# Kernel tuning notes

Hardware: AMD Instinct MI355X
Metric: run time of the kernel (lower is better)

## Reference

```python
import jax, jax.numpy as jnp
import numpy as np

B, H, W, C = 16, 56, 56, 384
WS, SHIFT, NH = 8, 4, 12
HID = 4 * C
N = WS * WS
EPS = 1e-5


def _rel_index():
    coords = np.stack(np.meshgrid(np.arange(WS), np.arange(WS), indexing='ij')).reshape(2, -1)
    rel = coords[:, :, None] - coords[:, None, :]
    rel = rel.transpose(1, 2, 0).astype(np.int32)
    rel[..., 0] += WS - 1
    rel[..., 1] += WS - 1
    rel[..., 0] *= 2 * WS - 1
    return rel.sum(-1)  # [N, N]


def _attn_mask():
    img = np.zeros((H, W))
    bounds = [(0, H - WS), (H - WS, H - SHIFT), (H - SHIFT, H)]
    cnt = 0
    for h0, h1 in bounds:
        for w0, w1 in bounds:
            img[h0:h1, w0:w1] = cnt
            cnt += 1
    mw = img.reshape(H // WS, WS, W // WS, WS).transpose(0, 2, 1, 3).reshape(-1, N)
    am = mw[:, None, :] - mw[:, :, None]
    return np.where(am != 0, -100.0, 0.0).astype(np.float32)  # [nW, N, N]


def setup_inputs() -> dict:
    key = jax.random.key(0)
    ks = jax.random.split(key, 12)
    s = lambda k, shp, sc=0.02: (jax.random.normal(k, shp, jnp.float32) * sc)
    return {
        'x': jax.random.normal(ks[0], (B, H * W, C), jnp.float32),
        'norm1_g': jnp.ones((C,), jnp.float32),
        'norm1_b': jnp.zeros((C,), jnp.float32),
        'qkv_w': s(ks[1], (C, 3 * C)),
        'qkv_b': jnp.zeros((3 * C,), jnp.float32),
        'proj_w': s(ks[2], (C, C)),
        'proj_b': jnp.zeros((C,), jnp.float32),
        'rel_bias': s(ks[3], ((2 * WS - 1) * (2 * WS - 1), NH)),
        'norm2_g': jnp.ones((C,), jnp.float32),
        'norm2_b': jnp.zeros((C,), jnp.float32),
        'fc1_w': s(ks[4], (C, HID)),
        'fc1_b': jnp.zeros((HID,), jnp.float32),
        'fc2_w': s(ks[5], (HID, C)),
        'fc2_b': jnp.zeros((C,), jnp.float32),
        'rel_index': jnp.asarray(_rel_index()),
        'attn_mask': jnp.asarray(_attn_mask()),
    }


def _ln(x, g, b):
    mu = x.mean(-1, keepdims=True)
    var = ((x - mu) ** 2).mean(-1, keepdims=True)
    return (x - mu) * jax.lax.rsqrt(var + EPS) * g + b


def reference(x, norm1_g, norm1_b, qkv_w, qkv_b, proj_w, proj_b, rel_bias,
              norm2_g, norm2_b, fc1_w, fc1_b, fc2_w, fc2_b, rel_index, attn_mask):
    hd = C // NH
    scale = hd ** -0.5
    shortcut = x
    h = _ln(x, norm1_g, norm1_b).reshape(B, H, W, C)
    h = jnp.roll(h, (-SHIFT, -SHIFT), axis=(1, 2))
    # window partition -> [B*nW, N, C]
    xw = h.reshape(B, H // WS, WS, W // WS, WS, C).transpose(0, 1, 3, 2, 4, 5).reshape(-1, N, C)
    B_ = xw.shape[0]
    qkv = (xw @ qkv_w + qkv_b).reshape(B_, N, 3, NH, hd).transpose(2, 0, 3, 1, 4)
    q, k, v = qkv[0], qkv[1], qkv[2]  # [B_, NH, N, hd]
    attn = jnp.einsum('bhid,bhjd->bhij', q * scale, k)
    bias = rel_bias[rel_index.reshape(-1)].reshape(N, N, NH).transpose(2, 0, 1)  # [NH, N, N]
    attn = attn + bias[None]
    nW = attn_mask.shape[0]
    attn = attn.reshape(B_ // nW, nW, NH, N, N) + attn_mask[None, :, None]
    attn = attn.reshape(B_, NH, N, N)
    attn = jax.nn.softmax(attn, axis=-1)
    out = jnp.einsum('bhij,bhjd->bhid', attn, v).transpose(0, 2, 1, 3).reshape(B_, N, C)
    out = out @ proj_w + proj_b
    # window reverse
    out = out.reshape(B, H // WS, W // WS, WS, WS, C).transpose(0, 1, 3, 2, 4, 5).reshape(B, H, W, C)
    out = jnp.roll(out, (SHIFT, SHIFT), axis=(1, 2)).reshape(B, H * W, C)
    y = shortcut + out
    h2 = _ln(y, norm2_g, norm2_b)
    mlp = jax.nn.gelu(h2 @ fc1_w + fc1_b, approximate=False) @ fc2_w + fc2_b
    y = y + mlp
    return (y, attn)
```

## Files before the change

### kernel.cpp

```cpp
#include <hip/hip_runtime.h>
#include <hip/hip_bf16.h>
#include <math.h>

#define ROWS 50176

typedef short s16;
typedef unsigned int u32;
typedef __attribute__((ext_vector_type(4))) float f32x4;
typedef __attribute__((ext_vector_type(8))) short s16x8;
typedef __attribute__((ext_vector_type(8))) __bf16 bf16x8;

typedef __attribute__((address_space(1))) const u32 gu32;
typedef __attribute__((address_space(3))) u32 lu32;

__device__ __forceinline__ void gload16(const void* g, void* l) {
  __builtin_amdgcn_global_load_lds((gu32*)g, (lu32*)l, 16, 0, 0);
}

__device__ __forceinline__ s16 f2bf(float f) {
  unsigned u = __float_as_uint(f);
  u = (u + 0x7fffu + ((u >> 16) & 1u)) >> 16;
  return (s16)u;
}

__global__ void convT(const float* __restrict__ src, s16* __restrict__ dst, int K, int N) {
  int i = blockIdx.x * 256 + threadIdx.x;
  if (i >= K * N) return;
  int n = i / K, k = i - n * K;
  dst[i] = f2bf(src[(size_t)k * N + n]);
}

__global__ __launch_bounds__(256) void ln_k(const float* __restrict__ x,
    const float* __restrict__ g, const float* __restrict__ b,
    s16* __restrict__ out, int window_map) {
  int r = blockIdx.x * 4 + (threadIdx.x >> 6);
  int lane = threadIdx.x & 63;
  size_t src;
  if (window_map) {
    int w = r >> 6, t = r & 63;
    int bb = w / 49, wi = w - bb * 49;
    int wh = wi / 7, ww = wi - wh * 7;
    int i = (wh * 8 + (t >> 3) + 4) % 56;
    int j = (ww * 8 + (t & 7) + 4) % 56;
    src = (size_t)bb * 3136 + i * 56 + j;
  } else {
    src = (size_t)r;
  }
  const float* xr = x + src * 384;
  float v[6];
  float s = 0.f;
#pragma unroll
  for (int e = 0; e < 6; ++e) { v[e] = xr[lane + e * 64]; s += v[e]; }
#pragma unroll
  for (int o = 1; o < 64; o <<= 1) s += __shfl_xor(s, o, 64);
  float mu = s * (1.f / 384.f);
  float q = 0.f;
#pragma unroll
  for (int e = 0; e < 6; ++e) { float d = v[e] - mu; q += d * d; }
#pragma unroll
  for (int o = 1; o < 64; o <<= 1) q += __shfl_xor(q, o, 64);
  float rs = rsqrtf(q * (1.f / 384.f) + 1e-5f);
  s16* orow = out + (size_t)r * 384;
#pragma unroll
  for (int e = 0; e < 6; ++e) {
    int c = lane + e * 64;
    orow[c] = f2bf((v[e] - mu) * rs * g[c] + b[c]);
  }
}

template<int EPI>
__global__ __launch_bounds__(256) void gemm_bt(const s16* __restrict__ A,
    const s16* __restrict__ BT, const float* __restrict__ bias, int K, int N,
    s16* __restrict__ obf, float* of, const float* res) {
  __shared__ s16 Asm[128 * 64];
  __shared__ s16 Bsm[128 * 64];
  const int t = threadIdx.x;
  const int nbx = N >> 7;
  const int nwg = gridDim.x;
  {
  }
  int id = blockIdx.x;
  const int q8 = nwg >> 3, r8 = nwg & 7;
  const int xcd = id & 7, loc = id >> 3;
  const int swz = (xcd < r8 ? xcd * (q8 + 1) : r8 * (q8 + 1) + (xcd - r8) * q8) + loc;
  const int by = swz / nbx, bx = swz - by * nbx;
  const int m0 = by * 128, n0 = bx * 128;

  const int wv = t >> 6, lane = t & 63;
  const int wr = wv >> 1, wc = wv & 1;
  const int lr = lane & 15, lg = lane >> 4;

  const s16* asrc[4]; const s16* bsrc[4];
  char* adst[4]; char* bdst[4];
#pragma unroll
  for (int i = 0; i < 4; ++i) {
    int o = (i * 256 + t) * 16;
    int row = o >> 7, pc = (o >> 4) & 7, lc = pc ^ (row & 7);
    asrc[i] = A + (size_t)(m0 + row) * K + lc * 8;
    adst[i] = (char*)Asm + o;
    bsrc[i] = BT + (size_t)(n0 + row) * K + lc * 8;
    bdst[i] = (char*)Bsm + o;
  }

  f32x4 acc[4][4] = {};

  for (int k0 = 0; k0 < K; k0 += 64) {
#pragma unroll
    for (int i = 0; i < 4; ++i) {
      gload16(asrc[i] + k0, adst[i]);
      gload16(bsrc[i] + k0, bdst[i]);
    }
    __syncthreads();
    bf16x8 af[2][4], bv[2][4];
#pragma unroll
    for (int kk = 0; kk < 2; ++kk) {
      const int cb = ((kk << 2) | lg) ^ (lr & 7);
#pragma unroll
      for (int m = 0; m < 4; ++m) {
        af[kk][m] = *reinterpret_cast<const bf16x8*>(
            (const char*)Asm + (wr * 64 + m * 16 + lr) * 128 + cb * 16);
        bv[kk][m] = *reinterpret_cast<const bf16x8*>(
            (const char*)Bsm + (wc * 64 + m * 16 + lr) * 128 + cb * 16);
      }
    }
#pragma unroll
    for (int kk = 0; kk < 2; ++kk)
#pragma unroll
      for (int m = 0; m < 4; ++m)
#pragma unroll
        for (int n = 0; n < 4; ++n)
          acc[m][n] = __builtin_amdgcn_mfma_f32_16x16x32_bf16(af[kk][m], bv[kk][n], acc[m][n], 0, 0, 0);
    __syncthreads();
  }

#pragma unroll
  for (int m = 0; m < 4; ++m) {
#pragma unroll
    for (int r = 0; r < 4; ++r) {
      const int row = m0 + wr * 64 + m * 16 + lg * 4 + r;
      size_t drow = (size_t)row;
      if (EPI == 1) {
        int w = row >> 6, tt = row & 63;
        int bb = w / 49, wi = w - bb * 49;
        int wh = wi / 7, ww = wi - wh * 7;
        int fi = (wh * 8 + (tt >> 3) + 4) % 56;
        int fj = (ww * 8 + (tt & 7) + 4) % 56;
        drow = (size_t)bb * 3136 + fi * 56 + fj;
      }
#pragma unroll
      for (int n = 0; n < 4; ++n) {
        const int col = n0 + wc * 64 + n * 16 + lr;
        float v = acc[m][n][r] + bias[col];
        if (EPI == 0) {
          obf[(size_t)row * N + col] = f2bf(v);
        } else if (EPI == 1) {
          size_t o = drow * 384 + col;
          of[o] = res[o] + v;
        } else if (EPI == 2) {
          v = 0.5f * v * (1.f + erff(v * 0.70710678118f));
          obf[(size_t)row * N + col] = f2bf(v);
        } else {
          size_t o = (size_t)row * 384 + col;
          of[o] = res[o] + v;
        }
      }
    }
  }
}

__global__ __launch_bounds__(64) void attn_k(const s16* __restrict__ qkv,
    const float* __restrict__ rel_bias, const int* __restrict__ rel_index,
    const float* __restrict__ mask, float* __restrict__ probs, s16* __restrict__ aout) {
  __shared__ s16 VT[32][72];
  __shared__ s16 P[64][72];
  const int blk = blockIdx.x;
  const int w = blk / 12, nh = blk - w * 12;
  const int lane = threadIdx.x;
  const int lr = lane & 15, lg = lane >> 4;
  const s16* base = qkv + (size_t)w * 64 * 1152;

  {
    const s16* vrow = base + (size_t)lane * 1152 + 768 + nh * 32;
    s16x8 v0 = *reinterpret_cast<const s16x8*>(vrow);
    s16x8 v1 = *reinterpret_cast<const s16x8*>(vrow + 8);
    s16x8 v2 = *reinterpret_cast<const s16x8*>(vrow + 16);
    s16x8 v3 = *reinterpret_cast<const s16x8*>(vrow + 24);
#pragma unroll
    for (int d = 0; d < 8; ++d) {
      VT[d][lane] = v0[d];
      VT[8 + d][lane] = v1[d];
      VT[16 + d][lane] = v2[d];
      VT[24 + d][lane] = v3[d];
    }
  }

  bf16x8 qf[4], kf[4];
#pragma unroll
  for (int m = 0; m < 4; ++m)
    qf[m] = *reinterpret_cast<const bf16x8*>(base + (size_t)(m * 16 + lr) * 1152 + nh * 32 + lg * 8);
#pragma unroll
  for (int n = 0; n < 4; ++n)
    kf[n] = *reinterpret_cast<const bf16x8*>(base + (size_t)(n * 16 + lr) * 1152 + 384 + nh * 32 + lg * 8);

  f32x4 s[4][4] = {};
#pragma unroll
  for (int m = 0; m < 4; ++m)
#pragma unroll
    for (int n = 0; n < 4; ++n)
      s[m][n] = __builtin_amdgcn_mfma_f32_16x16x32_bf16(qf[m], kf[n], s[m][n], 0, 0, 0);

  const float scale = 0.1767766952966369f;
  const float* mrow = mask + (size_t)(w % 49) * 4096;
#pragma unroll
  for (int m = 0; m < 4; ++m)
#pragma unroll
    for (int n = 0; n < 4; ++n)
#pragma unroll
      for (int r = 0; r < 4; ++r) {
        int i = m * 16 + lg * 4 + r, j = n * 16 + lr;
        s[m][n][r] = s[m][n][r] * scale
                   + rel_bias[(size_t)rel_index[i * 64 + j] * 12 + nh]
                   + mrow[i * 64 + j];
      }
#pragma unroll
  for (int m = 0; m < 4; ++m)
#pragma unroll
    for (int r = 0; r < 4; ++r) {
      float mx = fmaxf(fmaxf(s[m][0][r], s[m][1][r]), fmaxf(s[m][2][r], s[m][3][r]));
#pragma unroll
      for (int o = 1; o < 16; o <<= 1) mx = fmaxf(mx, __shfl_xor(mx, o, 64));
      float sum = 0.f;
#pragma unroll
      for (int n = 0; n < 4; ++n) {
        float e = __expf(s[m][n][r] - mx);
        s[m][n][r] = e;
        sum += e;
      }
#pragma unroll
      for (int o = 1; o < 16; o <<= 1) sum += __shfl_xor(sum, o, 64);
      float inv = 1.f / sum;
#pragma unroll
      for (int n = 0; n < 4; ++n) s[m][n][r] *= inv;
    }
  float* prow = probs + (size_t)(w * 12 + nh) * 4096;
#pragma unroll
  for (int m = 0; m < 4; ++m)
#pragma unroll
    for (int n = 0; n < 4; ++n)
#pragma unroll
      for (int r = 0; r < 4; ++r) {
        int i = m * 16 + lg * 4 + r, j = n * 16 + lr;
        float pv = s[m][n][r];
        prow[i * 64 + j] = pv;
        P[i][j] = f2bf(pv);
      }
  __syncthreads();
  f32x4 o2[4][2] = {};
#pragma unroll
  for (int m = 0; m < 4; ++m)
#pragma unroll
    for (int kk = 0; kk < 2; ++kk) {
      bf16x8 pa = *reinterpret_cast<const bf16x8*>(&P[m * 16 + lr][kk * 32 + lg * 8]);
#pragma unroll
      for (int n = 0; n < 2; ++n) {
        bf16x8 vb = *reinterpret_cast<const bf16x8*>(&VT[n * 16 + lr][kk * 32 + lg * 8]);
        o2[m][n] = __builtin_amdgcn_mfma_f32_16x16x32_bf16(pa, vb, o2[m][n], 0, 0, 0);
      }
    }
#pragma unroll
  for (int m = 0; m < 4; ++m)
#pragma unroll
    for (int n = 0; n < 2; ++n)
#pragma unroll
      for (int r = 0; r < 4; ++r) {
        int i = m * 16 + lg * 4 + r, d = n * 16 + lr;
        aout[((size_t)w * 64 + i) * 384 + nh * 32 + d] = f2bf(o2[m][n][r]);
      }
}

extern "C" void kernel_launch(void* const* d_in, const int* in_sizes, int n_in,
                              void* d_out, int out_size, void* d_ws, size_t ws_size,
                              hipStream_t stream) {
  const float* x        = (const float*)d_in[0];
  const float* n1g      = (const float*)d_in[1];
  const float* n1b      = (const float*)d_in[2];
  const float* qkv_w    = (const float*)d_in[3];
  const float* qkv_b    = (const float*)d_in[4];
  const float* proj_w   = (const float*)d_in[5];
  const float* proj_b   = (const float*)d_in[6];
  const float* rel_bias = (const float*)d_in[7];
  const float* n2g      = (const float*)d_in[8];
  const float* n2b      = (const float*)d_in[9];
  const float* fc1_w    = (const float*)d_in[10];
  const float* fc1_b    = (const float*)d_in[11];
  const float* fc2_w    = (const float*)d_in[12];
  const float* fc2_b    = (const float*)d_in[13];
  const int*   rel_idx  = (const int*)d_in[14];
  const float* amask    = (const float*)d_in[15];

  float* out   = (float*)d_out;
  float* probs = out + (size_t)ROWS * 384;

  s16* wqkvT = (s16*)d_ws;
  s16* wprojT = wqkvT + 1152 * 384;
  s16* wfc1T = wprojT + 384 * 384;
  s16* wfc2T = wfc1T + 1536 * 384;
  s16* bufA = wfc2T + 384 * 1536;
  s16* bufB = bufA + (size_t)ROWS * 384;
  s16* bufC = bufB + (size_t)ROWS * 1152;

  convT<<<(1152 * 384) / 256, 256, 0, stream>>>(qkv_w, wqkvT, 384, 1152);
  convT<<<(384 * 384) / 256, 256, 0, stream>>>(proj_w, wprojT, 384, 384);
  convT<<<(1536 * 384) / 256, 256, 0, stream>>>(fc1_w, wfc1T, 384, 1536);
  convT<<<(384 * 1536) / 256, 256, 0, stream>>>(fc2_w, wfc2T, 1536, 384);

  ln_k<<<ROWS / 4, 256, 0, stream>>>(x, n1g, n1b, bufA, 1);
  gemm_bt<0><<<(1152 / 128) * (ROWS / 128), 256, 0, stream>>>(bufA, wqkvT, qkv_b, 384, 1152, bufB, nullptr, nullptr);
  attn_k<<<784 * 12, 64, 0, stream>>>(bufB, rel_bias, rel_idx, amask, probs, bufC);
  gemm_bt<1><<<(384 / 128) * (ROWS / 128), 256, 0, stream>>>(bufC, wprojT, proj_b, 384, 384, nullptr, out, x);
  ln_k<<<ROWS / 4, 256, 0, stream>>>(out, n2g, n2b, bufA, 0);
  gemm_bt<2><<<(1536 / 128) * (ROWS / 128), 256, 0, stream>>>(bufA, wfc1T, fc1_b, 384, 1536, bufB, nullptr, nullptr);
  gemm_bt<3><<<(384 / 128) * (ROWS / 128), 256, 0, stream>>>(bufB, wfc2T, fc2_b, 1536, 384, nullptr, out, out);
}
```

Before: 547.8 us.

## Widen GEMM tiles to 128x192 with six waves, batch attention and weight conversion

The GEMM now uses 128x192 output tiles with 384 threads (2x3 waves) and a single shared buffer for the A and B tiles, which cuts the number of tiles and increases reuse of each A load. The attention kernel packs four window-head pairs per 256-thread block instead of one per 64-thread block. The four weight-transpose launches are merged into one. The wider GEMM tile adds register and LDS pressure and changes the number of workgroups per wave of dispatch. The epilogue lines not shown must also index columns for the 192-wide tile.

```diff
diff --git a/kernel.cpp b/kernel.cpp
--- a/kernel.cpp
+++ b/kernel.cpp
@@ -23,11 +23,18 @@
   return (s16)u;
 }
 
-__global__ void convT(const float* __restrict__ src, s16* __restrict__ dst, int K, int N) {
+__global__ __launch_bounds__(256) void convT_all(
+    const float* __restrict__ qkv_w, const float* __restrict__ proj_w,
+    const float* __restrict__ fc1_w, const float* __restrict__ fc2_w,
+    s16* __restrict__ wq, s16* __restrict__ wp, s16* __restrict__ w1, s16* __restrict__ w2) {
   int i = blockIdx.x * 256 + threadIdx.x;
-  if (i >= K * N) return;
-  int n = i / K, k = i - n * K;
-  dst[i] = f2bf(src[(size_t)k * N + n]);
+  const float* src; s16* dst; int K, N, off;
+  if (i < 442368)       { src = qkv_w;  dst = wq; K = 384;  N = 1152; off = i; }
+  else if (i < 589824)  { src = proj_w; dst = wp; K = 384;  N = 384;  off = i - 442368; }
+  else if (i < 1179648) { src = fc1_w;  dst = w1; K = 384;  N = 1536; off = i - 589824; }
+  else                  { src = fc2_w;  dst = w2; K = 1536; N = 384;  off = i - 1179648; }
+  int n = off / K, k = off - n * K;
+  dst[off] = f2bf(src[(size_t)k * N + n]);
 }
 
 __global__ __launch_bounds__(256) void ln_k(const float* __restrict__ x,
@@ -69,58 +76,57 @@
 }
 
 template<int EPI>
-__global__ __launch_bounds__(256) void gemm_bt(const s16* __restrict__ A,
+__global__ __launch_bounds__(384, 5) void gemm_bt(const s16* __restrict__ A,
     const s16* __restrict__ BT, const float* __restrict__ bias, int K, int N,
     s16* __restrict__ obf, float* of, const float* res) {
-  __shared__ s16 Asm[128 * 64];
-  __shared__ s16 Bsm[128 * 64];
+  __shared__ s16 smem[(128 + 192) * 64];
   const int t = threadIdx.x;
-  const int nbx = N >> 7;
+  const int nbx = N / 192;
   const int nwg = gridDim.x;
-  {
-  }
   int id = blockIdx.x;
   const int q8 = nwg >> 3, r8 = nwg & 7;
   const int xcd = id & 7, loc = id >> 3;
   const int swz = (xcd < r8 ? xcd * (q8 + 1) : r8 * (q8 + 1) + (xcd - r8) * q8) + loc;
   const int by = swz / nbx, bx = swz - by * nbx;
-  const int m0 = by * 128, n0 = bx * 128;
+  const int m0 = by * 128, n0 = bx * 192;
 
   const int wv = t >> 6, lane = t & 63;
-  const int wr = wv >> 1, wc = wv & 1;
+  const int wr = wv / 3, wc = wv - wr * 3;
   const int lr = lane & 15, lg = lane >> 4;
 
-  const s16* asrc[4]; const s16* bsrc[4];
-  char* adst[4]; char* bdst[4];
-#pragma unroll
-  for (int i = 0; i < 4; ++i) {
-    int o = (i * 256 + t) * 16;
-    int row = o >> 7, pc = (o >> 4) & 7, lc = pc ^ (row & 7);
-    asrc[i] = A + (size_t)(m0 + row) * K + lc * 8;
-    adst[i] = (char*)Asm + o;
-    bsrc[i] = BT + (size_t)(n0 + row) * K + lc * 8;
-    bdst[i] = (char*)Bsm + o;
+  const s16* gsrc[7]; int dofs[7];
+#pragma unroll
+  for (int i = 0; i < 7; ++i) {
+    int f = i * 384 + t;
+    if (f < 2560) {
+      int o = f * 16;
+      int row = o >> 7, pc = (o >> 4) & 7, lc = pc ^ (row & 7);
+      dofs[i] = o;
+      gsrc[i] = (row < 128 ? A + (size_t)(m0 + row) * K
+                           : BT + (size_t)(n0 + row - 128) * K) + lc * 8;
+    }
   }
 
   f32x4 acc[4][4] = {};
 
   for (int k0 = 0; k0 < K; k0 += 64) {
 #pragma unroll
-    for (int i = 0; i < 4; ++i) {
-      gload16(asrc[i] + k0, adst[i]);
-      gload16(bsrc[i] + k0, bdst[i]);
-    }
+    for (int i = 0; i < 6; ++i) gload16(gsrc[i] + k0, (char*)smem + dofs[i]);
+    if (t < 256) gload16(gsrc[6] + k0, (char*)smem + dofs[6]);
     __syncthreads();
+
+    const char* Ab = (const char*)smem;
+    const char* Bb = Ab + 128 * 128;
     bf16x8 af[2][4], bv[2][4];
 #pragma unroll
     for (int kk = 0; kk < 2; ++kk) {
-      const int cb = ((kk << 2) | lg) ^ (lr & 7);
+      const int cb = (kk << 2) | lg;
 #pragma unroll
       for (int m = 0; m < 4; ++m) {
-        af[kk][m] = *reinterpret_cast<const bf16x8*>(
-            (const char*)Asm + (wr * 64 + m * 16 + lr) * 128 + cb * 16);
-        bv[kk][m] = *reinterpret_cast<const bf16x8*>(
-            (const char*)Bsm + (wc * 64 + m * 16 + lr) * 128 + cb * 16);
+        int ar = wr * 64 + m * 16 + lr;
+        af[kk][m] = *reinterpret_cast<const bf16x8*>(Ab + ar * 128 + ((cb ^ (ar & 7)) * 16));
+        int br = wc * 64 + m * 16 + lr;
+        bv[kk][m] = *reinterpret_cast<const bf16x8*>(Bb + br * 128 + ((cb ^ (br & 7)) * 16));
       }
     }
 #pragma unroll
@@ -168,14 +174,15 @@
   }
 }
 
-__global__ __launch_bounds__(64) void attn_k(const s16* __restrict__ qkv,
+__global__ __launch_bounds__(256) void attn_k(const s16* __restrict__ qkv,
     const float* __restrict__ rel_bias, const int* __restrict__ rel_index,
     const float* __restrict__ mask, float* __restrict__ probs, s16* __restrict__ aout) {
-  __shared__ s16 VT[32][72];
-  __shared__ s16 P[64][72];
-  const int blk = blockIdx.x;
+  __shared__ s16 VT[4][32][72];
+  __shared__ s16 P[4][64][72];
+  const int u = threadIdx.x >> 6;
+  const int blk = blockIdx.x * 4 + u;
   const int w = blk / 12, nh = blk - w * 12;
-  const int lane = threadIdx.x;
+  const int lane = threadIdx.x & 63;
   const int lr = lane & 15, lg = lane >> 4;
   const s16* base = qkv + (size_t)w * 64 * 1152;
 
@@ -187,10 +194,10 @@
     s16x8 v3 = *reinterpret_cast<const s16x8*>(vrow + 24);
 #pragma unroll
     for (int d = 0; d < 8; ++d) {
-      VT[d][lane] = v0[d];
-      VT[8 + d][lane] = v1[d];
-      VT[16 + d][lane] = v2[d];
-      VT[24 + d][lane] = v3[d];
+      VT[u][d][lane] = v0[d];
+      VT[u][8 + d][lane] = v1[d];
+      VT[u][16 + d][lane] = v2[d];
+      VT[u][24 + d][lane] = v3[d];
     }
   }
 
@@ -252,7 +259,7 @@
         int i = m * 16 + lg * 4 + r, j = n * 16 + lr;
         float pv = s[m][n][r];
         prow[i * 64 + j] = pv;
-        P[i][j] = f2bf(pv);
+        P[u][i][j] = f2bf(pv);
       }
   __syncthreads();
   f32x4 o2[4][2] = {};
@@ -260,10 +267,10 @@
   for (int m = 0; m < 4; ++m)
 #pragma unroll
     for (int kk = 0; kk < 2; ++kk) {
-      bf16x8 pa = *reinterpret_cast<const bf16x8*>(&P[m * 16 + lr][kk * 32 + lg * 8]);
+      bf16x8 pa = *reinterpret_cast<const bf16x8*>(&P[u][m * 16 + lr][kk * 32 + lg * 8]);
 #pragma unroll
       for (int n = 0; n < 2; ++n) {
-        bf16x8 vb = *reinterpret_cast<const bf16x8*>(&VT[n * 16 + lr][kk * 32 + lg * 8]);
+        bf16x8 vb = *reinterpret_cast<const bf16x8*>(&VT[u][n * 16 + lr][kk * 32 + lg * 8]);
         o2[m][n] = __builtin_amdgcn_mfma_f32_16x16x32_bf16(pa, vb, o2[m][n], 0, 0, 0);
       }
     }
@@ -309,16 +316,13 @@
   s16* bufB = bufA + (size_t)ROWS * 384;
   s16* bufC = bufB + (size_t)ROWS * 1152;
 
-  convT<<<(1152 * 384) / 256, 256, 0, stream>>>(qkv_w, wqkvT, 384, 1152);
-  convT<<<(384 * 384) / 256, 256, 0, stream>>>(proj_w, wprojT, 384, 384);
-  convT<<<(1536 * 384) / 256, 256, 0, stream>>>(fc1_w, wfc1T, 384, 1536);
-  convT<<<(384 * 1536) / 256, 256, 0, stream>>>(fc2_w, wfc2T, 1536, 384);
+  convT_all<<<6912, 256, 0, stream>>>(qkv_w, proj_w, fc1_w, fc2_w, wqkvT, wprojT, wfc1T, wfc2T);
 
   ln_k<<<ROWS / 4, 256, 0, stream>>>(x, n1g, n1b, bufA, 1);
-  gemm_bt<0><<<(1152 / 128) * (ROWS / 128), 256, 0, stream>>>(bufA, wqkvT, qkv_b, 384, 1152, bufB, nullptr, nullptr);
-  attn_k<<<784 * 12, 64, 0, stream>>>(bufB, rel_bias, rel_idx, amask, probs, bufC);
-  gemm_bt<1><<<(384 / 128) * (ROWS / 128), 256, 0, stream>>>(bufC, wprojT, proj_b, 384, 384, nullptr, out, x);
+  gemm_bt<0><<<(1152 / 192) * (ROWS / 128), 384, 0, stream>>>(bufA, wqkvT, qkv_b, 384, 1152, bufB, nullptr, nullptr);
+  attn_k<<<784 * 12 / 4, 256, 0, stream>>>(bufB, rel_bias, rel_idx, amask, probs, bufC);
+  gemm_bt<1><<<(384 / 192) * (ROWS / 128), 384, 0, stream>>>(bufC, wprojT, proj_b, 384, 384, nullptr, out, x);
   ln_k<<<ROWS / 4, 256, 0, stream>>>(out, n2g, n2b, bufA, 0);
-  gemm_bt<2><<<(1536 / 128) * (ROWS / 128), 256, 0, stream>>>(bufA, wfc1T, fc1_b, 384, 1536, bufB, nullptr, nullptr);
-  gemm_bt<3><<<(384 / 128) * (ROWS / 128), 256, 0, stream>>>(bufB, wfc2T, fc2_b, 1536, 384, nullptr, out, out);
-}
+  gemm_bt<2><<<(1536 / 192) * (ROWS / 128), 384, 0, stream>>>(bufA, wfc1T, fc1_b, 384, 1536, bufB, nullptr, nullptr);
+  gemm_bt<3><<<(384 / 192) * (ROWS / 128), 384, 0, stream>>>(bufB, wfc2T, fc2_b, 1536, 384, nullptr, out, out);
+}
```

Result: slower. 1.095 ms (+99.9%).
